# Kernel tuning notes

Hardware: AMD Instinct MI355X
Metric: run time of the kernel (lower is better)

The kernel has to match this reference:

```python
import jax, jax.numpy as jnp
import numpy as np

# MACE-style symmetric contraction, correlation = 3
# x: [n, C, I] mul_ir features; indices: [n] species ids
# U^{(nu)}: generalized (symmetrized) Clebsch-Gordan tensors (constant buffers)
#   u3: [D, I, I, I, P3], u2: [D, I, I, P2], u1: [D, I, P1]
# w^{(nu)}: per-element basis weights [E, P_nu, C]
N, C, I, D, E = 4096, 128, 9, 9, 10
P3, P2, P1 = 23, 5, 3


def setup_inputs() -> dict:
    key = jax.random.key(0)
    ks = jax.random.split(key, 8)
    x = jax.random.normal(ks[0], (N, C, I), dtype=jnp.float32)
    indices = jax.random.randint(ks[1], (N,), 0, E, dtype=jnp.int64)
    # CG coupling tensors are sparse constants in the real module; we use
    # deterministic dense stand-ins with the correct shapes/contraction pattern.
    u3 = jax.random.normal(ks[2], (D, I, I, I, P3), dtype=jnp.float32) * 0.1
    u2 = jax.random.normal(ks[3], (D, I, I, P2), dtype=jnp.float32) * 0.1
    u1 = jax.random.normal(ks[4], (D, I, P1), dtype=jnp.float32) * 0.1
    w3 = jax.random.normal(ks[5], (E, P3, C), dtype=jnp.float32) * 0.1
    w2 = jax.random.normal(ks[6], (E, P2, C), dtype=jnp.float32) * 0.1
    w1 = jax.random.normal(ks[7], (E, P1, C), dtype=jnp.float32) * 0.1
    return {"x": x, "indices": indices, "u3": u3, "u2": u2, "u1": u1,
            "w3": w3, "w2": w2, "w1": w1}


def reference(x, indices, u3, u2, u1, w3, w2, w1):
    # gather per-node basis weights by species (irregular gather)
    w3g = w3[indices]  # [n, P3, C]
    w2g = w2[indices]  # [n, P2, C]
    w1g = w1[indices]  # [n, P1, C]
    # highest correlation order: contract one copy of x
    out = jnp.einsum('dijkp,bpc,bck->bcdij', u3, w3g, x)  # [n, C, D, I, I]
    # order 2: add coupling, contract another copy of x
    c2 = jnp.einsum('dijp,bpc->bcdij', u2, w2g) + out
    out = jnp.einsum('bcdij,bcj->bcdi', c2, x)            # [n, C, D, I]
    # order 1: add coupling, contract final copy of x
    c1 = jnp.einsum('dip,bpc->bcdi', u1, w1g) + out
    out = jnp.einsum('bcdi,bci->bcd', c1, x)              # [n, C, D]
    return out
```

## Files before the change

kernel.cpp:

```cpp
#include <hip/hip_runtime.h>

#define NN 4096
#define CC 128
#define II 9
#define DD 9
#define EE 10
#define PP3 23
#define PP2 5
#define PP1 3
#define F3 165
#define F2 45
#define F1 9
#define FTOT (F3 + F2 + F1)
#define FPAD 224
#define NKT14 14

#define SU3_ELEMS (F3 * PP3 * DD)
#define SU2_ELEMS (F2 * PP2 * DD)
#define SU3_OFF 0
#define SU2_OFF (SU3_OFF + SU3_ELEMS * 4)
#define CUR_OFF (SU2_OFF + SU2_ELEMS * 4)
#define LIST_OFF (CUR_OFF + 64)
#define WG16_OFF (LIST_OFF + NN * EE * 4)

#define CPB 4
#define TS 8
#define WFD 64
#define SYMN (F3 * PP3 * 9 + F2 * PP2 * 9)
#define SYMBLK ((SYMN + 255) / 256)

typedef _Float16 f16x8 __attribute__((ext_vector_type(8)));
typedef __fp16 fp16x2 __attribute__((ext_vector_type(2)));
typedef float f32x16 __attribute__((ext_vector_type(16)));

static __device__ __forceinline__ unsigned pkrtz(float a, float b) {
    fp16x2 h = __builtin_amdgcn_cvt_pkrtz(a, b);
    return __builtin_bit_cast(unsigned, h);
}

static __device__ __forceinline__ unsigned short h16(float a) {
    _Float16 ha = (_Float16)a;
    return __builtin_bit_cast(unsigned short, ha);
}

__global__ void prep_kernel(const float* __restrict__ u3,
                            const float* __restrict__ u2,
                            float* __restrict__ su3,
                            float* __restrict__ su2,
                            const int* __restrict__ indices,
                            int* __restrict__ cursors,
                            int* __restrict__ lists) {
    if (blockIdx.x < SYMBLK) {
        const int gid = blockIdx.x * 256 + threadIdx.x;
        if (gid < F3 * PP3 * 9) {
            const int t = gid / (PP3 * 9);
            const int rr = gid % (PP3 * 9);
            const int p = rr / 9;
            const int d = rr % 9;
            int I0 = 0, J0 = 0, K0 = 0;
            {
                int rem = t;
                bool found = false;
                for (int i = 0; i < 9 && !found; i++)
                    for (int j = i; j < 9 && !found; j++) {
                        int cnt = 9 - j;
                        if (rem < cnt) { I0 = i; J0 = j; K0 = j + rem; found = true; }
                        else rem -= cnt;
                    }
            }
            int a[3] = {I0, J0, K0};
            const int ord[6][3] = {{0,1,2},{0,2,1},{1,0,2},{1,2,0},{2,0,1},{2,1,0}};
            int codes[6];
            int np = 0;
            float s = 0.f;
            for (int q = 0; q < 6; q++) {
                int ii = a[ord[q][0]], jj = a[ord[q][1]], kk = a[ord[q][2]];
                int code = (ii * 9 + jj) * 9 + kk;
                bool seen = false;
                for (int r = 0; r < np; r++) if (codes[r] == code) seen = true;
                if (!seen) {
                    codes[np++] = code;
                    s += u3[(((((d * 9 + ii) * 9 + jj) * 9 + kk)) * PP3) + p];
                }
            }
            su3[(t * PP3 + p) * 9 + d] = s;
        } else if (gid < SYMN) {
            const int g2 = gid - F3 * PP3 * 9;
            const int t = g2 / (PP2 * 9);
            const int rr = g2 % (PP2 * 9);
            const int p = rr / 9;
            const int d = rr % 9;
            int I0 = 0, J0 = 0;
            {
                int rem = t;
                bool found = false;
                for (int i = 0; i < 9 && !found; i++) {
                    int cnt = 9 - i;
                    if (rem < cnt) { I0 = i; J0 = i + rem; found = true; }
                    else rem -= cnt;
                }
            }
            float s = u2[(((d * 9 + I0) * 9 + J0) * PP2) + p];
            if (I0 != J0) s += u2[(((d * 9 + J0) * 9 + I0) * PP2) + p];
            su2[(t * PP2 + p) * 9 + d] = s;
        }
    } else {
        const int b = (blockIdx.x - SYMBLK) * 256 + threadIdx.x;
        if (b < NN) {
            const int e = indices[b];
            const int slot = atomicAdd(&cursors[e], 1);
            lists[e * NN + slot] = b;
        }
    }
}

__global__ __launch_bounds__(256) void wprep_v3_kernel(
    const float* __restrict__ su3,
    const float* __restrict__ su2,
    const float* __restrict__ u1,
    const float* __restrict__ w3,
    const float* __restrict__ w2,
    const float* __restrict__ w1,
    unsigned short* __restrict__ Wg16)
{
    const int e = blockIdx.y;
    const int fd0 = blockIdx.x * WFD;
    const int c = threadIdx.x & 127;
    const int sub = threadIdx.x >> 7;

    __shared__ float sW3[PP3 * CC];
    __shared__ float sW2[PP2 * CC];
    __shared__ float sW1[PP1 * CC];
    __shared__ unsigned short sT[CC * 66];

    for (int q = threadIdx.x; q < PP3 * CC; q += 256) sW3[q] = w3[e * PP3 * CC + q];
    for (int q = threadIdx.x; q < PP2 * CC; q += 256) sW2[q] = w2[e * PP2 * CC + q];
    for (int q = threadIdx.x; q < PP1 * CC; q += 256) sW1[q] = w1[e * PP1 * CC + q];
    __syncthreads();

    #pragma unroll
    for (int it = 0; it < WFD / 2; it++) {
        const int l = it * 2 + sub;
        const int fd = fd0 + l;
        const int d = fd / FPAD;
        const int f = fd - d * FPAD;
        float v = 0.f;
        if (d < 9) {
            if (f < F3) {
                #pragma unroll
                for (int p = 0; p < PP3; p++)
                    v += su3[(f * PP3 + p) * 9 + d] * sW3[p * CC + c];
            } else if (f < F3 + F2) {
                #pragma unroll
                for (int p = 0; p < PP2; p++)
                    v += su2[((f - F3) * PP2 + p) * 9 + d] * sW2[p * CC + c];
            } else if (f < FTOT) {
                #pragma unroll
                for (int p = 0; p < PP1; p++)
                    v += u1[(d * 9 + (f - F3 - F2)) * PP1 + p] * sW1[p * CC + c];
            }
        }
        sT[c * 66 + l] = h16(v);
    }
    __syncthreads();

    unsigned* dst = reinterpret_cast<unsigned*>(Wg16);
    for (int q = threadIdx.x; q < CC * 32; q += 256) {
        const int cc = q >> 5;
        const int dw = q & 31;
        if (fd0 + dw * 2 < 9 * FPAD) {
            const unsigned lo = sT[cc * 66 + dw * 2];
            const unsigned hi = sT[cc * 66 + dw * 2 + 1];
            dst[(size_t)(e * CC + cc) * (9 * FPAD / 2) + fd0 / 2 + dw] = lo | (hi << 16);
        }
    }
}

__global__ __launch_bounds__(256, 4) void symcon_reg32_kernel(
    const float* __restrict__ x,
    const unsigned short* __restrict__ Wg16,
    const int* __restrict__ cursors,
    const int* __restrict__ lists,
    float* __restrict__ out)
{
    const int e = blockIdx.y;
    const int lane = threadIdx.x & 63;
    const int wid = threadIdx.x >> 6;
    const int c = blockIdx.x * CPB + wid;
    const int r = lane & 31;
    const int g = lane >> 5;
    const bool isg1 = (g == 1);

    f16x8 bfrag[NKT14];
    {
        const unsigned short* wp = Wg16 + (size_t)(e * CC + c) * (9 * FPAD);
        #pragma unroll
        for (int t = 0; t < NKT14; t++) {
            f16x8 v = {0, 0, 0, 0, 0, 0, 0, 0};
            if (r < 9)
                v = *reinterpret_cast<const f16x8*>(wp + r * FPAD + t * 16 + g * 8);
            bfrag[t] = v;
        }
    }

    const int cnt = cursors[e];
    const int ntiles = (cnt + 31) >> 5;
    const int* lbase = lists + e * NN;
    float* outc = out + (size_t)c * DD;

    int T = blockIdx.z;
    int nb_cur, nb_next;
    float xv[9];
    {
        const int n = T * 32 + r;
        const bool valid = (T < ntiles) && (n < cnt);
        nb_cur = valid ? lbase[n] : 0;
        const float* xr = x + ((size_t)nb_cur * CC + c) * II;
        #pragma unroll
        for (int q = 0; q < 9; q++) xv[q] = valid ? xr[q] : 0.f;
    }
    {
        const int n = (T + TS) * 32 + r;
        const bool valid = (T + TS < ntiles) && (n < cnt);
        nb_next = valid ? lbase[n] : 0;
    }

    while (T < ntiles) {
        float xn[9];
        {
            const int n = (T + TS) * 32 + r;
            const bool valid = (T + TS < ntiles) && (n < cnt);
            const float* xr = x + ((size_t)nb_next * CC + c) * II;
            #pragma unroll
            for (int q = 0; q < 9; q++) xn[q] = valid ? xr[q] : 0.f;
        }
        int nb_next2;
        {
            const int n = (T + 2 * TS) * 32 + r;
            const bool valid = (T + 2 * TS < ntiles) && (n < cnt);
            nb_next2 = valid ? lbase[n] : 0;
        }

        f32x16 acc = {0.f, 0.f, 0.f, 0.f, 0.f, 0.f, 0.f, 0.f,
                      0.f, 0.f, 0.f, 0.f, 0.f, 0.f, 0.f, 0.f};
        unsigned au[4];
        {
            float pend = 0.f;
            int F = 0;
#define EMITR(expr) { const float _m = (expr);                                \
            if (F & 1) { const unsigned _pk = pkrtz(pend, _m);                \
                const int _P = F >> 1; const int _t = _P >> 3;                \
                const int _q = _P & 7; const int _jd = _q & 3;                \
                if (_q < 4) au[_jd] = _pk;                                    \
                else        au[_jd] = isg1 ? _pk : au[_jd];                   \
                if (_q == 7) {                                                \
                    f16x8 af;                                                 \
                    unsigned* _ap = reinterpret_cast<unsigned*>(&af);         \
                    _ap[0] = au[0]; _ap[1] = au[1];                           \
                    _ap[2] = au[2]; _ap[3] = au[3];                           \
                    acc = __builtin_amdgcn_mfma_f32_32x32x16_f16(             \
                        af, bfrag[_t], acc, 0, 0, 0);                         \
                }                                                             \
            } else pend = _m; F++; }
            #pragma unroll
            for (int i = 0; i < 9; i++)
                #pragma unroll
                for (int j = i; j < 9; j++) {
                    const float xij = xv[i] * xv[j];
                    #pragma unroll
                    for (int k = j; k < 9; k++)
                        EMITR(xij * xv[k])
                }
            #pragma unroll
            for (int i = 0; i < 9; i++)
                #pragma unroll
                for (int j = i; j < 9; j++)
                    EMITR(xv[i] * xv[j])
            #pragma unroll
            for (int i = 0; i < 9; i++)
                EMITR(xv[i])
            #pragma unroll
            for (int z = 0; z < 5; z++)
                EMITR(0.f)
#undef EMITR
        }

        #pragma unroll
        for (int reg = 0; reg < 16; reg++) {
            const int row = (reg & 3) + 8 * (reg >> 2) + 4 * g;
            const int sb = __shfl(nb_cur, row);
            const int slot = T * 32 + row;
            if (r < 9 && slot < cnt)
                outc[(size_t)sb * (CC * DD) + r] = acc[reg];
        }

        #pragma unroll
        for (int q = 0; q < 9; q++) xv[q] = xn[q];
        nb_cur = nb_next;
        nb_next = nb_next2;
        T += TS;
    }
}

extern "C" void kernel_launch(void* const* d_in, const int* in_sizes, int n_in,
                              void* d_out, int out_size, void* d_ws, size_t ws_size,
                              hipStream_t stream) {
    const float* x   = (const float*)d_in[0];
    const int* indices = (const int*)d_in[1];
    const float* u3  = (const float*)d_in[2];
    const float* u2  = (const float*)d_in[3];
    const float* u1  = (const float*)d_in[4];
    const float* w3  = (const float*)d_in[5];
    const float* w2  = (const float*)d_in[6];
    const float* w1  = (const float*)d_in[7];
    float* out = (float*)d_out;

    char* ws = (char*)d_ws;
    float* su3 = (float*)(ws + SU3_OFF);
    float* su2 = (float*)(ws + SU2_OFF);
    int* cursors = (int*)(ws + CUR_OFF);
    int* lists = (int*)(ws + LIST_OFF);
    unsigned short* Wg16 = (unsigned short*)(ws + WG16_OFF);

    hipMemsetAsync(cursors, 0, 64, stream);
    hipLaunchKernelGGL(prep_kernel, dim3(SYMBLK + (NN + 255) / 256), dim3(256), 0, stream,
                       u3, u2, su3, su2, indices, cursors, lists);
    hipLaunchKernelGGL(wprep_v3_kernel, dim3((9 * FPAD + WFD - 1) / WFD, EE),
                       dim3(256), 0, stream, su3, su2, u1, w3, w2, w1, Wg16);
    hipLaunchKernelGGL(symcon_reg32_kernel, dim3(CC / CPB, EE, TS), dim3(256), 0, stream,
                       x, Wg16, cursors, lists, out);
}
```

Measured before the change: 103.3 us.

## Fuse prep, weight-prep and contraction kernels into one cooperative persistent kernel

```diff
diff --git a/kernel.cpp b/kernel.cpp
--- a/kernel.cpp
+++ b/kernel.cpp
@@ -1,4 +1,7 @@
 #include <hip/hip_runtime.h>
+#include <hip/hip_cooperative_groups.h>
+
+namespace cg = cooperative_groups;
 
 #define NN 4096
 #define CC 128
@@ -25,9 +28,9 @@
 
 #define CPB 4
 #define TS 8
-#define WFD 64
+#define NUNITS (32 * EE * TS)
+#define WUNITS (126 * EE)
 #define SYMN (F3 * PP3 * 9 + F2 * PP2 * 9)
-#define SYMBLK ((SYMN + 255) / 256)
 
 typedef _Float16 f16x8 __attribute__((ext_vector_type(8)));
 typedef __fp16 fp16x2 __attribute__((ext_vector_type(2)));
@@ -43,15 +46,29 @@
     return __builtin_bit_cast(unsigned short, ha);
 }
 
-__global__ void prep_kernel(const float* __restrict__ u3,
-                            const float* __restrict__ u2,
-                            float* __restrict__ su3,
-                            float* __restrict__ su2,
-                            const int* __restrict__ indices,
-                            int* __restrict__ cursors,
-                            int* __restrict__ lists) {
-    if (blockIdx.x < SYMBLK) {
-        const int gid = blockIdx.x * 256 + threadIdx.x;
+__global__ __launch_bounds__(256, 4) void mega_kernel(
+    const float* __restrict__ x,
+    const float* __restrict__ u3,
+    const float* __restrict__ u2,
+    const float* __restrict__ u1,
+    const float* __restrict__ w3,
+    const float* __restrict__ w2,
+    const float* __restrict__ w1,
+    const int* __restrict__ indices,
+    float* __restrict__ su3,
+    float* __restrict__ su2,
+    int* __restrict__ cursors,
+    int* __restrict__ lists,
+    unsigned short* __restrict__ Wg16,
+    float* __restrict__ out)
+{
+    cg::grid_group gg = cg::this_grid();
+    const int tid = threadIdx.x;
+    const int nblk = gridDim.x;
+
+    __shared__ unsigned short sT[CC * 18];
+
+    for (int gid = blockIdx.x * 256 + tid; gid < SYMN + NN; gid += nblk * 256) {
         if (gid < F3 * PP3 * 9) {
             const int t = gid / (PP3 * 9);
             const int rr = gid % (PP3 * 9);
@@ -103,202 +120,180 @@
             float s = u2[(((d * 9 + I0) * 9 + J0) * PP2) + p];
             if (I0 != J0) s += u2[(((d * 9 + J0) * 9 + I0) * PP2) + p];
             su2[(t * PP2 + p) * 9 + d] = s;
-        }
-    } else {
-        const int b = (blockIdx.x - SYMBLK) * 256 + threadIdx.x;
-        if (b < NN) {
+        } else {
+            const int b = gid - SYMN;
             const int e = indices[b];
             const int slot = atomicAdd(&cursors[e], 1);
             lists[e * NN + slot] = b;
         }
     }
-}
-
-__global__ __launch_bounds__(256) void wprep_v3_kernel(
-    const float* __restrict__ su3,
-    const float* __restrict__ su2,
-    const float* __restrict__ u1,
-    const float* __restrict__ w3,
-    const float* __restrict__ w2,
-    const float* __restrict__ w1,
-    unsigned short* __restrict__ Wg16)
-{
-    const int e = blockIdx.y;
-    const int fd0 = blockIdx.x * WFD;
-    const int c = threadIdx.x & 127;
-    const int sub = threadIdx.x >> 7;
-
-    __shared__ float sW3[PP3 * CC];
-    __shared__ float sW2[PP2 * CC];
-    __shared__ float sW1[PP1 * CC];
-    __shared__ unsigned short sT[CC * 66];
-
-    for (int q = threadIdx.x; q < PP3 * CC; q += 256) sW3[q] = w3[e * PP3 * CC + q];
-    for (int q = threadIdx.x; q < PP2 * CC; q += 256) sW2[q] = w2[e * PP2 * CC + q];
-    for (int q = threadIdx.x; q < PP1 * CC; q += 256) sW1[q] = w1[e * PP1 * CC + q];
-    __syncthreads();
-
-    #pragma unroll
-    for (int it = 0; it < WFD / 2; it++) {
-        const int l = it * 2 + sub;
-        const int fd = fd0 + l;
-        const int d = fd / FPAD;
-        const int f = fd - d * FPAD;
-        float v = 0.f;
-        if (d < 9) {
-            if (f < F3) {
-                #pragma unroll
-                for (int p = 0; p < PP3; p++)
-                    v += su3[(f * PP3 + p) * 9 + d] * sW3[p * CC + c];
-            } else if (f < F3 + F2) {
-                #pragma unroll
-                for (int p = 0; p < PP2; p++)
-                    v += su2[((f - F3) * PP2 + p) * 9 + d] * sW2[p * CC + c];
-            } else if (f < FTOT) {
-                #pragma unroll
-                for (int p = 0; p < PP1; p++)
-                    v += u1[(d * 9 + (f - F3 - F2)) * PP1 + p] * sW1[p * CC + c];
-            }
-        }
-        sT[c * 66 + l] = h16(v);
+    gg.sync();
+
+    for (int unit = blockIdx.x; unit < WUNITS; unit += nblk) {
+        const int e = unit / 126;
+        const int fd0 = (unit % 126) * 16;
+        const int c = tid & 127;
+        const int sub = tid >> 7;
+        #pragma unroll
+        for (int it = 0; it < 8; it++) {
+            const int l = it * 2 + sub;
+            const int fd = fd0 + l;
+            const int d = fd / FPAD;
+            const int f = fd - d * FPAD;
+            float v = 0.f;
+            if (d < 9) {
+                if (f < F3) {
+                    #pragma unroll
+                    for (int p = 0; p < PP3; p++)
+                        v += su3[(f * PP3 + p) * 9 + d] * w3[(e * PP3 + p) * CC + c];
+                } else if (f < F3 + F2) {
+                    #pragma unroll
+                    for (int p = 0; p < PP2; p++)
+                        v += su2[((f - F3) * PP2 + p) * 9 + d] * w2[(e * PP2 + p) * CC + c];
+                } else if (f < FTOT) {
+                    #pragma unroll
+                    for (int p = 0; p < PP1; p++)
+                        v += u1[(d * 9 + (f - F3 - F2)) * PP1 + p] * w1[(e * PP1 + p) * CC + c];
+                }
+            }
+            sT[c * 18 + l] = h16(v);
+        }
+        __syncthreads();
+        unsigned* dst = reinterpret_cast<unsigned*>(Wg16);
+        for (int q = tid; q < CC * 8; q += 256) {
+            const int cc = q >> 3;
+            const int dw = q & 7;
+            const unsigned lo = sT[cc * 18 + dw * 2];
+            const unsigned hi = sT[cc * 18 + dw * 2 + 1];
+            dst[(size_t)(e * CC + cc) * (9 * FPAD / 2) + fd0 / 2 + dw] = lo | (hi << 16);
+        }
+        __syncthreads();
     }
-    __syncthreads();
-
-    unsigned* dst = reinterpret_cast<unsigned*>(Wg16);
-    for (int q = threadIdx.x; q < CC * 32; q += 256) {
-        const int cc = q >> 5;
-        const int dw = q & 31;
-        if (fd0 + dw * 2 < 9 * FPAD) {
-            const unsigned lo = sT[cc * 66 + dw * 2];
-            const unsigned hi = sT[cc * 66 + dw * 2 + 1];
-            dst[(size_t)(e * CC + cc) * (9 * FPAD / 2) + fd0 / 2 + dw] = lo | (hi << 16);
-        }
-    }
-}
-
-__global__ __launch_bounds__(256, 4) void symcon_reg32_kernel(
-    const float* __restrict__ x,
-    const unsigned short* __restrict__ Wg16,
-    const int* __restrict__ cursors,
-    const int* __restrict__ lists,
-    float* __restrict__ out)
-{
-    const int e = blockIdx.y;
-    const int lane = threadIdx.x & 63;
-    const int wid = threadIdx.x >> 6;
-    const int c = blockIdx.x * CPB + wid;
+    gg.sync();
+
+    const int lane = tid & 63;
+    const int wid = tid >> 6;
     const int r = lane & 31;
     const int g = lane >> 5;
     const bool isg1 = (g == 1);
 
-    f16x8 bfrag[NKT14];
-    {
-        const unsigned short* wp = Wg16 + (size_t)(e * CC + c) * (9 * FPAD);
-        #pragma unroll
-        for (int t = 0; t < NKT14; t++) {
-            f16x8 v = {0, 0, 0, 0, 0, 0, 0, 0};
-            if (r < 9)
-                v = *reinterpret_cast<const f16x8*>(wp + r * FPAD + t * 16 + g * 8);
-            bfrag[t] = v;
-        }
-    }
-
-    const int cnt = cursors[e];
-    const int ntiles = (cnt + 31) >> 5;
-    const int* lbase = lists + e * NN;
-    float* outc = out + (size_t)c * DD;
-
-    int T = blockIdx.z;
-    int nb_cur, nb_next;
-    float xv[9];
-    {
-        const int n = T * 32 + r;
-        const bool valid = (T < ntiles) && (n < cnt);
-        nb_cur = valid ? lbase[n] : 0;
-        const float* xr = x + ((size_t)nb_cur * CC + c) * II;
-        #pragma unroll
-        for (int q = 0; q < 9; q++) xv[q] = valid ? xr[q] : 0.f;
-    }
-    {
-        const int n = (T + TS) * 32 + r;
-        const bool valid = (T + TS < ntiles) && (n < cnt);
-        nb_next = valid ? lbase[n] : 0;
-    }
-
-    while (T < ntiles) {
-        float xn[9];
+    for (int unit = blockIdx.x; unit < NUNITS; unit += nblk) {
+        const int bx = unit & 31;
+        const int e = (unit >> 5) % EE;
+        const int z = unit / (32 * EE);
+        const int c = bx * CPB + wid;
+
+        const int cnt = cursors[e];
+        const int ntiles = (cnt + 31) >> 5;
+        if (z >= ntiles) continue;
+
+        f16x8 bfrag[NKT14];
+        {
+            const unsigned short* wp = Wg16 + (size_t)(e * CC + c) * (9 * FPAD);
+            #pragma unroll
+            for (int t = 0; t < NKT14; t++) {
+                f16x8 v = {0, 0, 0, 0, 0, 0, 0, 0};
+                if (r < 9)
+                    v = *reinterpret_cast<const f16x8*>(wp + r * FPAD + t * 16 + g * 8);
+                bfrag[t] = v;
+            }
+        }
+
+        const int* lbase = lists + e * NN;
+        float* outc = out + (size_t)c * DD;
+
+        int T = z;
+        int nb_cur, nb_next;
+        float xv[9];
+        {
+            const int n = T * 32 + r;
+            const bool valid = (n < cnt);
+            nb_cur = valid ? lbase[n] : 0;
+            const float* xr = x + ((size_t)nb_cur * CC + c) * II;
+            #pragma unroll
+            for (int q = 0; q < 9; q++) xv[q] = valid ? xr[q] : 0.f;
+        }
         {
             const int n = (T + TS) * 32 + r;
             const bool valid = (T + TS < ntiles) && (n < cnt);
-            const float* xr = x + ((size_t)nb_next * CC + c) * II;
+            nb_next = valid ? lbase[n] : 0;
+        }
+
+        while (T < ntiles) {
+            float xn[9];
+            {
+                const int n = (T + TS) * 32 + r;
+                const bool valid = (T + TS < ntiles) && (n < cnt);
+                const float* xr = x + ((size_t)nb_next * CC + c) * II;
+                #pragma unroll
+                for (int q = 0; q < 9; q++) xn[q] = valid ? xr[q] : 0.f;
+            }
+            int nb_next2;
+            {
+                const int n = (T + 2 * TS) * 32 + r;
+                const bool valid = (T + 2 * TS < ntiles) && (n < cnt);
+                nb_next2 = valid ? lbase[n] : 0;
+            }
+
+            f32x16 acc = {0.f, 0.f, 0.f, 0.f, 0.f, 0.f, 0.f, 0.f,
+                          0.f, 0.f, 0.f, 0.f, 0.f, 0.f, 0.f, 0.f};
+            unsigned au[4];
+            {
+                float pend = 0.f;
+                int F = 0;
+#define EMITR(expr) { const float _m = (expr);                                \
+                if (F & 1) { const unsigned _pk = pkrtz(pend, _m);            \
+                    const int _P = F >> 1; const int _t = _P >> 3;            \
+                    const int _q = _P & 7; const int _jd = _q & 3;            \
+                    if (_q < 4) au[_jd] = _pk;                                \
+                    else        au[_jd] = isg1 ? _pk : au[_jd];               \
+                    if (_q == 7) {                                            \
+                        f16x8 af;                                             \
+                        unsigned* _ap = reinterpret_cast<unsigned*>(&af);     \
+                        _ap[0] = au[0]; _ap[1] = au[1];                       \
+                        _ap[2] = au[2]; _ap[3] = au[3];                       \
+                        acc = __builtin_amdgcn_mfma_f32_32x32x16_f16(         \
+                            af, bfrag[_t], acc, 0, 0, 0);                     \
+                    }                                                         \
+                } else pend = _m; F++; }
+                #pragma unroll
+                for (int i = 0; i < 9; i++)
+                    #pragma unroll
+                    for (int j = i; j < 9; j++) {
+                        const float xij = xv[i] * xv[j];
+                        #pragma unroll
+                        for (int k = j; k < 9; k++)
+                            EMITR(xij * xv[k])
+                    }
+                #pragma unroll
+                for (int i = 0; i < 9; i++)
+                    #pragma unroll
+                    for (int j = i; j < 9; j++)
+                        EMITR(xv[i] * xv[j])
+                #pragma unroll
+                for (int i = 0; i < 9; i++)
+                    EMITR(xv[i])
+                #pragma unroll
+                for (int z2 = 0; z2 < 5; z2++)
+                    EMITR(0.f)
+#undef EMITR
+            }
+
             #pragma unroll
-            for (int q = 0; q < 9; q++) xn[q] = valid ? xr[q] : 0.f;
-        }
-        int nb_next2;
-        {
-            const int n = (T + 2 * TS) * 32 + r;
-            const bool valid = (T + 2 * TS < ntiles) && (n < cnt);
-            nb_next2 = valid ? lbase[n] : 0;
-        }
-
-        f32x16 acc = {0.f, 0.f, 0.f, 0.f, 0.f, 0.f, 0.f, 0.f,
-                      0.f, 0.f, 0.f, 0.f, 0.f, 0.f, 0.f, 0.f};
-        unsigned au[4];
-        {
-            float pend = 0.f;
-            int F = 0;
-#define EMITR(expr) { const float _m = (expr);                                \
-            if (F & 1) { const unsigned _pk = pkrtz(pend, _m);                \
-                const int _P = F >> 1; const int _t = _P >> 3;                \
-                const int _q = _P & 7; const int _jd = _q & 3;                \
-                if (_q < 4) au[_jd] = _pk;                                    \
-                else        au[_jd] = isg1 ? _pk : au[_jd];                   \
-                if (_q == 7) {                                                \
-                    f16x8 af;                                                 \
-                    unsigned* _ap = reinterpret_cast<unsigned*>(&af);         \
-                    _ap[0] = au[0]; _ap[1] = au[1];                           \
-                    _ap[2] = au[2]; _ap[3] = au[3];                           \
-                    acc = __builtin_amdgcn_mfma_f32_32x32x16_f16(             \
-                        af, bfrag[_t], acc, 0, 0, 0);                         \
-                }                                                             \
-            } else pend = _m; F++; }
+            for (int reg = 0; reg < 16; reg++) {
+                const int row = (reg & 3) + 8 * (reg >> 2) + 4 * g;
+                const int sb = __shfl(nb_cur, row);
+                const int slot = T * 32 + row;
+                if (r < 9 && slot < cnt)
+                    outc[(size_t)sb * (CC * DD) + r] = acc[reg];
+            }
+
             #pragma unroll
-            for (int i = 0; i < 9; i++)
-                #pragma unroll
-                for (int j = i; j < 9; j++) {
-                    const float xij = xv[i] * xv[j];
-                    #pragma unroll
-                    for (int k = j; k < 9; k++)
-                        EMITR(xij * xv[k])
-                }
-            #pragma unroll
-            for (int i = 0; i < 9; i++)
-                #pragma unroll
-                for (int j = i; j < 9; j++)
-                    EMITR(xv[i] * xv[j])
-            #pragma unroll
-            for (int i = 0; i < 9; i++)
-                EMITR(xv[i])
-            #pragma unroll
-            for (int z = 0; z < 5; z++)
-                EMITR(0.f)
-#undef EMITR
-        }
-
-        #pragma unroll
-        for (int reg = 0; reg < 16; reg++) {
-            const int row = (reg & 3) + 8 * (reg >> 2) + 4 * g;
-            const int sb = __shfl(nb_cur, row);
-            const int slot = T * 32 + row;
-            if (r < 9 && slot < cnt)
-                outc[(size_t)sb * (CC * DD) + r] = acc[reg];
-        }
-
-        #pragma unroll
-        for (int q = 0; q < 9; q++) xv[q] = xn[q];
-        nb_cur = nb_next;
-        nb_next = nb_next2;
-        T += TS;
+            for (int q = 0; q < 9; q++) xv[q] = xn[q];
+            nb_cur = nb_next;
+            nb_next = nb_next2;
+            T += TS;
+        }
     }
 }
 
@@ -323,10 +318,17 @@
     unsigned short* Wg16 = (unsigned short*)(ws + WG16_OFF);
 
     hipMemsetAsync(cursors, 0, 64, stream);
-    hipLaunchKernelGGL(prep_kernel, dim3(SYMBLK + (NN + 255) / 256), dim3(256), 0, stream,
-                       u3, u2, su3, su2, indices, cursors, lists);
-    hipLaunchKernelGGL(wprep_v3_kernel, dim3((9 * FPAD + WFD - 1) / WFD, EE),
-                       dim3(256), 0, stream, su3, su2, u1, w3, w2, w1, Wg16);
-    hipLaunchKernelGGL(symcon_reg32_kernel, dim3(CC / CPB, EE, TS), dim3(256), 0, stream,
-                       x, Wg16, cursors, lists, out);
+
+    int maxb = 0;
+    hipOccupancyMaxActiveBlocksPerMultiprocessor(&maxb, (const void*)mega_kernel, 256, 0);
+    if (maxb < 1) maxb = 1;
+    int gridsz = 256 * maxb;
+    if (gridsz > 960) gridsz = 960;
+
+    void* args[] = {(void*)&x, (void*)&u3, (void*)&u2, (void*)&u1,
+                    (void*)&w3, (void*)&w2, (void*)&w1, (void*)&indices,
+                    (void*)&su3, (void*)&su2, (void*)&cursors, (void*)&lists,
+                    (void*)&Wg16, (void*)&out};
+    hipLaunchCooperativeKernel((void*)mega_kernel, dim3(gridsz), dim3(256),
+                               args, 0, stream);
 }
```

After: 250.7 us. +142.8%, slower.

## Fuse U symmetrization and weight-contraction prep into a single kernel

Applied to the files above, without the earlier changes.

```diff
diff --git a/kernel.cpp b/kernel.cpp
--- a/kernel.cpp
+++ b/kernel.cpp
@@ -15,19 +15,13 @@
 #define FPAD 224
 #define NKT14 14
 
-#define SU3_ELEMS (F3 * PP3 * DD)
-#define SU2_ELEMS (F2 * PP2 * DD)
-#define SU3_OFF 0
-#define SU2_OFF (SU3_OFF + SU3_ELEMS * 4)
-#define CUR_OFF (SU2_OFF + SU2_ELEMS * 4)
+#define CUR_OFF 0
 #define LIST_OFF (CUR_OFF + 64)
 #define WG16_OFF (LIST_OFF + NN * EE * 4)
 
 #define CPB 4
 #define TS 8
-#define WFD 64
-#define SYMN (F3 * PP3 * 9 + F2 * PP2 * 9)
-#define SYMBLK ((SYMN + 255) / 256)
+#define WBLK 126
 
 typedef _Float16 f16x8 __attribute__((ext_vector_type(8)));
 typedef __fp16 fp16x2 __attribute__((ext_vector_type(2)));
@@ -43,28 +37,48 @@
     return __builtin_bit_cast(unsigned short, ha);
 }
 
-__global__ void prep_kernel(const float* __restrict__ u3,
-                            const float* __restrict__ u2,
-                            float* __restrict__ su3,
-                            float* __restrict__ su2,
-                            const int* __restrict__ indices,
-                            int* __restrict__ cursors,
-                            int* __restrict__ lists) {
-    if (blockIdx.x < SYMBLK) {
-        const int gid = blockIdx.x * 256 + threadIdx.x;
-        if (gid < F3 * PP3 * 9) {
-            const int t = gid / (PP3 * 9);
-            const int rr = gid % (PP3 * 9);
-            const int p = rr / 9;
-            const int d = rr % 9;
+__global__ __launch_bounds__(256) void prep_kernel(
+    const float* __restrict__ u3,
+    const float* __restrict__ u2,
+    const float* __restrict__ u1,
+    const float* __restrict__ w3,
+    const float* __restrict__ w2,
+    const float* __restrict__ w1,
+    const int* __restrict__ indices,
+    int* __restrict__ cursors,
+    int* __restrict__ lists,
+    unsigned short* __restrict__ Wg16)
+{
+    const int tid = threadIdx.x;
+    if (blockIdx.x >= WBLK) {
+        const int b = (blockIdx.x - WBLK) * 256 + tid;
+        if (b < NN) {
+            const int e = indices[b];
+            const int slot = atomicAdd(&cursors[e], 1);
+            lists[e * NN + slot] = b;
+        }
+        return;
+    }
+
+    const int fd0 = blockIdx.x * 16;
+    __shared__ float sSu[16 * 23];
+    __shared__ unsigned short sT[2 * CC * 18];
+
+    for (int idx = tid; idx < 16 * 23; idx += 256) {
+        const int l = idx / 23, p = idx % 23;
+        const int fd = fd0 + l;
+        const int d = fd / FPAD;
+        const int f = fd - d * FPAD;
+        float s = 0.f;
+        if (f < F3) {
             int I0 = 0, J0 = 0, K0 = 0;
             {
-                int rem = t;
-                bool found = false;
-                for (int i = 0; i < 9 && !found; i++)
-                    for (int j = i; j < 9 && !found; j++) {
+                int rem = f;
+                bool fo = false;
+                for (int i = 0; i < 9 && !fo; i++)
+                    for (int j = i; j < 9 && !fo; j++) {
                         int cnt = 9 - j;
-                        if (rem < cnt) { I0 = i; J0 = j; K0 = j + rem; found = true; }
+                        if (rem < cnt) { I0 = i; J0 = j; K0 = j + rem; fo = true; }
                         else rem -= cnt;
                     }
             }
@@ -72,107 +86,85 @@
             const int ord[6][3] = {{0,1,2},{0,2,1},{1,0,2},{1,2,0},{2,0,1},{2,1,0}};
             int codes[6];
             int np = 0;
-            float s = 0.f;
             for (int q = 0; q < 6; q++) {
                 int ii = a[ord[q][0]], jj = a[ord[q][1]], kk = a[ord[q][2]];
                 int code = (ii * 9 + jj) * 9 + kk;
                 bool seen = false;
-                for (int r = 0; r < np; r++) if (codes[r] == code) seen = true;
+                for (int r2 = 0; r2 < np; r2++) if (codes[r2] == code) seen = true;
                 if (!seen) {
                     codes[np++] = code;
-                    s += u3[(((((d * 9 + ii) * 9 + jj) * 9 + kk)) * PP3) + p];
+                    s += u3[((((d * 9 + ii) * 9 + jj) * 9 + kk)) * PP3 + p];
                 }
             }
-            su3[(t * PP3 + p) * 9 + d] = s;
-        } else if (gid < SYMN) {
-            const int g2 = gid - F3 * PP3 * 9;
-            const int t = g2 / (PP2 * 9);
-            const int rr = g2 % (PP2 * 9);
-            const int p = rr / 9;
-            const int d = rr % 9;
-            int I0 = 0, J0 = 0;
-            {
-                int rem = t;
-                bool found = false;
-                for (int i = 0; i < 9 && !found; i++) {
-                    int cnt = 9 - i;
-                    if (rem < cnt) { I0 = i; J0 = i + rem; found = true; }
-                    else rem -= cnt;
+        } else if (f < F3 + F2) {
+            if (p < PP2) {
+                const int t2 = f - F3;
+                int I0 = 0, J0 = 0;
+                {
+                    int rem = t2;
+                    bool fo = false;
+                    for (int i = 0; i < 9 && !fo; i++) {
+                        int cnt = 9 - i;
+                        if (rem < cnt) { I0 = i; J0 = i + rem; fo = true; }
+                        else rem -= cnt;
+                    }
                 }
+                s = u2[(((d * 9 + I0) * 9 + J0) * PP2) + p];
+                if (I0 != J0) s += u2[(((d * 9 + J0) * 9 + I0) * PP2) + p];
             }
-            float s = u2[(((d * 9 + I0) * 9 + J0) * PP2) + p];
-            if (I0 != J0) s += u2[(((d * 9 + J0) * 9 + I0) * PP2) + p];
-            su2[(t * PP2 + p) * 9 + d] = s;
-        }
-    } else {
-        const int b = (blockIdx.x - SYMBLK) * 256 + threadIdx.x;
-        if (b < NN) {
-            const int e = indices[b];
-            const int slot = atomicAdd(&cursors[e], 1);
-            lists[e * NN + slot] = b;
-        }
-    }
-}
-
-__global__ __launch_bounds__(256) void wprep_v3_kernel(
-    const float* __restrict__ su3,
-    const float* __restrict__ su2,
-    const float* __restrict__ u1,
-    const float* __restrict__ w3,
-    const float* __restrict__ w2,
-    const float* __restrict__ w1,
-    unsigned short* __restrict__ Wg16)
-{
-    const int e = blockIdx.y;
-    const int fd0 = blockIdx.x * WFD;
-    const int c = threadIdx.x & 127;
-    const int sub = threadIdx.x >> 7;
-
-    __shared__ float sW3[PP3 * CC];
-    __shared__ float sW2[PP2 * CC];
-    __shared__ float sW1[PP1 * CC];
-    __shared__ unsigned short sT[CC * 66];
-
-    for (int q = threadIdx.x; q < PP3 * CC; q += 256) sW3[q] = w3[e * PP3 * CC + q];
-    for (int q = threadIdx.x; q < PP2 * CC; q += 256) sW2[q] = w2[e * PP2 * CC + q];
-    for (int q = threadIdx.x; q < PP1 * CC; q += 256) sW1[q] = w1[e * PP1 * CC + q];
+        } else if (f < FTOT) {
+            if (p < PP1) s = u1[(d * 9 + (f - F3 - F2)) * PP1 + p];
+        }
+        sSu[idx] = s;
+    }
     __syncthreads();
 
-    #pragma unroll
-    for (int it = 0; it < WFD / 2; it++) {
-        const int l = it * 2 + sub;
-        const int fd = fd0 + l;
-        const int d = fd / FPAD;
-        const int f = fd - d * FPAD;
-        float v = 0.f;
-        if (d < 9) {
+    const int c = tid & 127;
+    const int sub = tid >> 7;
+    unsigned* dst = reinterpret_cast<unsigned*>(Wg16);
+
+    for (int eit = 0; eit < 5; eit++) {
+        const int e = eit * 2 + sub;
+        float wv3[PP3];
+        #pragma unroll
+        for (int p = 0; p < PP3; p++) wv3[p] = w3[(e * PP3 + p) * CC + c];
+        float wv2[PP2];
+        #pragma unroll
+        for (int p = 0; p < PP2; p++) wv2[p] = w2[(e * PP2 + p) * CC + c];
+        float wv1[PP1];
+        #pragma unroll
+        for (int p = 0; p < PP1; p++) wv1[p] = w1[(e * PP1 + p) * CC + c];
+
+        #pragma unroll
+        for (int l = 0; l < 16; l++) {
+            const int fd = fd0 + l;
+            const int d = fd / FPAD;
+            const int f = fd - d * FPAD;
+            float v = 0.f;
             if (f < F3) {
                 #pragma unroll
-                for (int p = 0; p < PP3; p++)
-                    v += su3[(f * PP3 + p) * 9 + d] * sW3[p * CC + c];
+                for (int p = 0; p < PP3; p++) v += sSu[l * 23 + p] * wv3[p];
             } else if (f < F3 + F2) {
                 #pragma unroll
-                for (int p = 0; p < PP2; p++)
-                    v += su2[((f - F3) * PP2 + p) * 9 + d] * sW2[p * CC + c];
+                for (int p = 0; p < PP2; p++) v += sSu[l * 23 + p] * wv2[p];
             } else if (f < FTOT) {
                 #pragma unroll
-                for (int p = 0; p < PP1; p++)
-                    v += u1[(d * 9 + (f - F3 - F2)) * PP1 + p] * sW1[p * CC + c];
+                for (int p = 0; p < PP1; p++) v += sSu[l * 23 + p] * wv1[p];
             }
-        }
-        sT[c * 66 + l] = h16(v);
-    }
-    __syncthreads();
-
-    unsigned* dst = reinterpret_cast<unsigned*>(Wg16);
-    for (int q = threadIdx.x; q < CC * 32; q += 256) {
-        const int cc = q >> 5;
-        const int dw = q & 31;
-        if (fd0 + dw * 2 < 9 * FPAD) {
-            const unsigned lo = sT[cc * 66 + dw * 2];
-            const unsigned hi = sT[cc * 66 + dw * 2 + 1];
-            dst[(size_t)(e * CC + cc) * (9 * FPAD / 2) + fd0 / 2 + dw] = lo | (hi << 16);
-        }
+            sT[(sub * CC + c) * 18 + l] = h16(v);
+        }
+        __syncthreads();
+
+        for (int q = tid; q < 2 * CC * 8; q += 256) {
+            const int se = q >> 10;
+            const int cc = (q >> 3) & 127;
+            const int dw = q & 7;
+            const int ee = eit * 2 + se;
+            const unsigned lo = sT[(se * CC + cc) * 18 + dw * 2];
+            const unsigned hi = sT[(se * CC + cc) * 18 + dw * 2 + 1];
+            dst[(size_t)(ee * CC + cc) * (9 * FPAD / 2) + fd0 / 2 + dw] = lo | (hi << 16);
+        }
+        __syncthreads();
     }
 }
 
@@ -316,17 +308,13 @@
     float* out = (float*)d_out;
 
     char* ws = (char*)d_ws;
-    float* su3 = (float*)(ws + SU3_OFF);
-    float* su2 = (float*)(ws + SU2_OFF);
     int* cursors = (int*)(ws + CUR_OFF);
     int* lists = (int*)(ws + LIST_OFF);
     unsigned short* Wg16 = (unsigned short*)(ws + WG16_OFF);
 
     hipMemsetAsync(cursors, 0, 64, stream);
-    hipLaunchKernelGGL(prep_kernel, dim3(SYMBLK + (NN + 255) / 256), dim3(256), 0, stream,
-                       u3, u2, su3, su2, indices, cursors, lists);
-    hipLaunchKernelGGL(wprep_v3_kernel, dim3((9 * FPAD + WFD - 1) / WFD, EE),
-                       dim3(256), 0, stream, su3, su2, u1, w3, w2, w1, Wg16);
+    hipLaunchKernelGGL(prep_kernel, dim3(WBLK + (NN + 255) / 256), dim3(256), 0, stream,
+                       u3, u2, u1, w3, w2, w1, indices, cursors, lists, Wg16);
     hipLaunchKernelGGL(symcon_reg32_kernel, dim3(CC / CPB, EE, TS), dim3(256), 0, stream,
                        x, Wg16, cursors, lists, out);
 }
```

New measurement: 97.78 us. -5.3%, faster.
